# Performance work log

Measured on AMD Instinct MI355X. Metric: run time of the kernel, lower is better.

The kernel has to match this reference:

```python
import jax, jax.numpy as jnp
import numpy as np

B, H, K, V = 64, 32, 128, 128


def setup_inputs() -> dict:
    key = jax.random.key(0)
    ks = jax.random.split(key, 7)
    q = jax.random.normal(ks[0], (B, 1, H, K), dtype=jnp.float32)
    k = jax.random.normal(ks[1], (B, 1, H, K), dtype=jnp.float32)
    v = jax.random.normal(ks[2], (B, 1, H, V), dtype=jnp.float32)
    # a = -kappa, b = kappa*a_gate in RWKV-7; plain gaussians suffice for a math reference
    a = jax.random.normal(ks[3], (B, 1, H, K), dtype=jnp.float32)
    b = jax.random.normal(ks[4], (B, 1, H, K), dtype=jnp.float32)
    # gk is a log-decay: negative so exp(gk) in (0, 1]
    gk = -jnp.abs(jax.random.normal(ks[5], (B, 1, H, K), dtype=jnp.float32)) * 0.1
    h0 = jax.random.normal(ks[6], (B, H, K, V), dtype=jnp.float32) * 0.1
    return {"q": q, "k": k, "v": v, "a": a, "b": b, "gk": gk, "h0": h0}


def reference(q, k, v, a, b, gk, h0):
    """RWKV-7 DPLR single-step (T=1) decode recurrence, per (batch, head):
      g     = exp(gk)                                # [K] decay
      s     = a^T H0                                 # [V]
      t     = (q*g)^T H0                             # [V]
      alpha = q . b ; beta = q . k                   # scalars
      o     = t + alpha*s + beta*v                   # [V]
      Ht    = diag(g) H0 + b s^T + k v^T             # [K,V]
    Mirrors dplr_decode_t1_kernel_streamK exactly (fp32 accumulation).
    """
    qf = q[:, 0].astype(jnp.float32)   # [B,H,K]
    kf = k[:, 0].astype(jnp.float32)
    af = a[:, 0].astype(jnp.float32)
    bf = b[:, 0].astype(jnp.float32)
    vf = v[:, 0].astype(jnp.float32)   # [B,H,V]
    g = jnp.exp(gk[:, 0].astype(jnp.float32))  # [B,H,K]
    hf = h0.astype(jnp.float32)        # [B,H,K,V]

    s = jnp.einsum('bhk,bhkv->bhv', af, hf)
    t = jnp.einsum('bhk,bhkv->bhv', qf * g, hf)
    alpha = jnp.sum(qf * bf, axis=-1, keepdims=True)  # [B,H,1]
    beta = jnp.sum(qf * kf, axis=-1, keepdims=True)   # [B,H,1]
    o = t + alpha * s + beta * vf                      # [B,H,V]

    ht = g[..., None] * hf + bf[..., None] * s[:, :, None, :] + kf[..., None] * vf[:, :, None, :]
    return o[:, None].astype(v.dtype), ht.astype(h0.dtype)
```

## Files before the change

### kernel.cpp

```cpp
#include <hip/hip_runtime.h>


#define KD 128
#define VD 128
#define BH_TOTAL 2048
#define WPB 4
#define NBLK (BH_TOTAL/WPB)
#define RKEEP 16
#define NSTRM (64 - RKEEP)

typedef float f32x4 __attribute__((ext_vector_type(4)));

__global__ __launch_bounds__(256, 2) void dplr_decode_wave_kernel(
    const float* __restrict__ q_,  const float* __restrict__ k_,
    const float* __restrict__ v_,  const float* __restrict__ a_,
    const float* __restrict__ b_,  const float* __restrict__ gk_,
    const float* __restrict__ h0_, float* __restrict__ out_)
{
    const int tid  = threadIdx.x;
    const int wid  = tid >> 6;
    const int lane = tid & 63;
    const int bh   = blockIdx.x * WPB + wid;
    const int half = lane >> 5;
    const int c4   = (lane & 31) * 4;

    const size_t vec_off = (size_t)bh * KD;
    const size_t h_off   = (size_t)bh * (KD * VD);

    __shared__ float aL[WPB][2][64], qgL[WPB][2][64], gL[WPB][2][64],
                     bL[WPB][2][64], kL[WPB][2][64];

    const float q_lo = q_[vec_off + lane],  q_hi = q_[vec_off + lane + 64];
    const float b_lo = b_[vec_off + lane],  b_hi = b_[vec_off + lane + 64];
    const float k_lo = k_[vec_off + lane],  k_hi = k_[vec_off + lane + 64];
    const float a_lo = a_[vec_off + lane],  a_hi = a_[vec_off + lane + 64];
    const float g_lo = expf(gk_[vec_off + lane]);
    const float g_hi = expf(gk_[vec_off + lane + 64]);

    {
        const int p  = lane & 1;
        const int m0 = lane >> 1;
        aL [wid][p][m0] = a_lo;        aL [wid][p][m0 + 32] = a_hi;
        qgL[wid][p][m0] = q_lo * g_lo; qgL[wid][p][m0 + 32] = q_hi * g_hi;
        gL [wid][p][m0] = g_lo;        gL [wid][p][m0 + 32] = g_hi;
        bL [wid][p][m0] = b_lo;        bL [wid][p][m0 + 32] = b_hi;
        kL [wid][p][m0] = k_lo;        kL [wid][p][m0 + 32] = k_hi;
    }

    float alpha = q_lo * b_lo + q_hi * b_hi;
    float beta  = q_lo * k_lo + q_hi * k_hi;
#pragma unroll
    for (int o = 32; o > 0; o >>= 1) {
        alpha += __shfl_xor(alpha, o, 64);
        beta  += __shfl_xor(beta,  o, 64);
    }

    const f32x4 v4 = *(const f32x4*)(v_ + vec_off + c4);

    const float* hp = h0_ + h_off + (size_t)half * VD + c4;

    f32x4 sp = {0.f, 0.f, 0.f, 0.f};
    f32x4 tp = {0.f, 0.f, 0.f, 0.f};
    f32x4 Hk[RKEEP];

#pragma unroll
    for (int mb = 0; mb < NSTRM / 4; ++mb) {
        const f32x4 av = *(const f32x4*)&aL [wid][half][mb * 4];
        const f32x4 qv = *(const f32x4*)&qgL[wid][half][mb * 4];
#pragma unroll
        for (int e = 0; e < 4; ++e) {
            const int m = mb * 4 + e;
            const f32x4 h = *(const f32x4*)(hp + (size_t)m * 256);
            sp += av[e] * h;
            tp += qv[e] * h;
        }
    }
#pragma unroll
    for (int j = 0; j < RKEEP; ++j) {
        const int m = NSTRM + j;
        Hk[j] = *(const f32x4*)(hp + (size_t)m * 256);
        sp += aL [wid][half][m] * Hk[j];
        tp += qgL[wid][half][m] * Hk[j];
    }

    f32x4 s4, t4;
#pragma unroll
    for (int e = 0; e < 4; ++e) {
        s4[e] = sp[e] + __shfl_xor(sp[e], 32, 64);
        t4[e] = tp[e] + __shfl_xor(tp[e], 32, 64);
    }

    if (half == 0) {
        const f32x4 o4 = t4 + alpha * s4 + beta * v4;
        *(f32x4*)(out_ + (size_t)bh * VD + c4) = o4;
    }

    float* op = out_ + (size_t)BH_TOTAL * VD + h_off + (size_t)half * VD + c4;
#pragma unroll
    for (int mb = 0; mb < NSTRM / 4; ++mb) {
        const f32x4 gv = *(const f32x4*)&gL[wid][half][mb * 4];
        const f32x4 bv = *(const f32x4*)&bL[wid][half][mb * 4];
        const f32x4 kv = *(const f32x4*)&kL[wid][half][mb * 4];
#pragma unroll
        for (int e = 0; e < 4; ++e) {
            const int m = mb * 4 + e;
            const f32x4 h = __builtin_nontemporal_load((const f32x4*)(hp + (size_t)m * 256));
            const f32x4 o4 = gv[e] * h + bv[e] * s4 + kv[e] * v4;
            __builtin_nontemporal_store(o4, (f32x4*)(op + (size_t)m * 256));
        }
    }
#pragma unroll
    for (int j = 0; j < RKEEP; ++j) {
        const int m = NSTRM + j;
        const f32x4 o4 = gL[wid][half][m] * Hk[j] + bL[wid][half][m] * s4
                       + kL[wid][half][m] * v4;
        __builtin_nontemporal_store(o4, (f32x4*)(op + (size_t)m * 256));
    }
}

extern "C" void kernel_launch(void* const* d_in, const int* in_sizes, int n_in,
                              void* d_out, int out_size, void* d_ws, size_t ws_size,
                              hipStream_t stream) {
    const float* q  = (const float*)d_in[0];
    const float* k  = (const float*)d_in[1];
    const float* v  = (const float*)d_in[2];
    const float* a  = (const float*)d_in[3];
    const float* b  = (const float*)d_in[4];
    const float* gk = (const float*)d_in[5];
    const float* h0 = (const float*)d_in[6];
    float* out = (float*)d_out;

    dplr_decode_wave_kernel<<<NBLK, 256, 0, stream>>>(q, k, v, a, b, gk, h0, out);
}
```

Measured before the change: 254.4 us.

## Split each head's state across a whole block by column groups

Each (batch, head) pair now gets its own 256-thread block instead of one wave. Each wave owns 32 value columns, and 8 row groups per wave cover 16 rows each; the s and t partial sums are reduced with a three-step shuffle. The register cache of the last 16 rows is removed, so the second pass re-reads all of H0 with ordinary cached loads instead of nontemporal ones, and the occupancy hint is raised. The aim is more memory parallelism and occupancy, at the cost of re-reading the full state, which now depends on L2 hits.

New measurement: 254.7 us. About the same (+0.1%).

```diff
diff --git a/kernel.cpp b/kernel.cpp
--- a/kernel.cpp
+++ b/kernel.cpp
@@ -5,13 +5,11 @@
 #define VD 128
 #define BH_TOTAL 2048
 #define WPB 4
-#define NBLK (BH_TOTAL/WPB)
-#define RKEEP 16
-#define NSTRM (64 - RKEEP)
+#define NBLK BH_TOTAL
 
 typedef float f32x4 __attribute__((ext_vector_type(4)));
 
-__global__ __launch_bounds__(256, 2) void dplr_decode_wave_kernel(
+__global__ __launch_bounds__(256, 6) void dplr_decode_colsplit_kernel(
     const float* __restrict__ q_,  const float* __restrict__ k_,
     const float* __restrict__ v_,  const float* __restrict__ a_,
     const float* __restrict__ b_,  const float* __restrict__ gk_,
@@ -20,15 +18,16 @@
     const int tid  = threadIdx.x;
     const int wid  = tid >> 6;
     const int lane = tid & 63;
-    const int bh   = blockIdx.x * WPB + wid;
-    const int half = lane >> 5;
-    const int c4   = (lane & 31) * 4;
+    const int bh   = blockIdx.x;
+    const int rg   = lane >> 3;
+    const int l8   = lane & 7;
+    const int c4   = wid * 32 + l8 * 4;
 
     const size_t vec_off = (size_t)bh * KD;
     const size_t h_off   = (size_t)bh * (KD * VD);
 
-    __shared__ float aL[WPB][2][64], qgL[WPB][2][64], gL[WPB][2][64],
-                     bL[WPB][2][64], kL[WPB][2][64];
+    __shared__ float aL[WPB][8][16], qgL[WPB][8][16], gL[WPB][8][16],
+                     bL[WPB][8][16], kL[WPB][8][16];
 
     const float q_lo = q_[vec_off + lane],  q_hi = q_[vec_off + lane + 64];
     const float b_lo = b_[vec_off + lane],  b_hi = b_[vec_off + lane + 64];
@@ -38,13 +37,13 @@
     const float g_hi = expf(gk_[vec_off + lane + 64]);
 
     {
-        const int p  = lane & 1;
-        const int m0 = lane >> 1;
-        aL [wid][p][m0] = a_lo;        aL [wid][p][m0 + 32] = a_hi;
-        qgL[wid][p][m0] = q_lo * g_lo; qgL[wid][p][m0 + 32] = q_hi * g_hi;
-        gL [wid][p][m0] = g_lo;        gL [wid][p][m0 + 32] = g_hi;
-        bL [wid][p][m0] = b_lo;        bL [wid][p][m0 + 32] = b_hi;
-        kL [wid][p][m0] = k_lo;        kL [wid][p][m0 + 32] = k_hi;
+        const int p  = lane & 7;
+        const int m0 = lane >> 3;
+        aL [wid][p][m0] = a_lo;        aL [wid][p][m0 + 8] = a_hi;
+        qgL[wid][p][m0] = q_lo * g_lo; qgL[wid][p][m0 + 8] = q_hi * g_hi;
+        gL [wid][p][m0] = g_lo;        gL [wid][p][m0 + 8] = g_hi;
+        bL [wid][p][m0] = b_lo;        bL [wid][p][m0 + 8] = b_hi;
+        kL [wid][p][m0] = k_lo;        kL [wid][p][m0 + 8] = k_hi;
     }
 
     float alpha = q_lo * b_lo + q_hi * b_hi;
@@ -57,64 +56,56 @@
 
     const f32x4 v4 = *(const f32x4*)(v_ + vec_off + c4);
 
-    const float* hp = h0_ + h_off + (size_t)half * VD + c4;
+    const float* hp = h0_ + h_off + (size_t)rg * VD + c4;
 
     f32x4 sp = {0.f, 0.f, 0.f, 0.f};
     f32x4 tp = {0.f, 0.f, 0.f, 0.f};
-    f32x4 Hk[RKEEP];
-
 #pragma unroll
-    for (int mb = 0; mb < NSTRM / 4; ++mb) {
-        const f32x4 av = *(const f32x4*)&aL [wid][half][mb * 4];
-        const f32x4 qv = *(const f32x4*)&qgL[wid][half][mb * 4];
+    for (int mb = 0; mb < 4; ++mb) {
+        const f32x4 av = *(const f32x4*)&aL [wid][rg][mb * 4];
+        const f32x4 qv = *(const f32x4*)&qgL[wid][rg][mb * 4];
 #pragma unroll
         for (int e = 0; e < 4; ++e) {
             const int m = mb * 4 + e;
-            const f32x4 h = *(const f32x4*)(hp + (size_t)m * 256);
+            const f32x4 h = *(const f32x4*)(hp + (size_t)m * (8 * VD));
             sp += av[e] * h;
             tp += qv[e] * h;
         }
-    }
-#pragma unroll
-    for (int j = 0; j < RKEEP; ++j) {
-        const int m = NSTRM + j;
-        Hk[j] = *(const f32x4*)(hp + (size_t)m * 256);
-        sp += aL [wid][half][m] * Hk[j];
-        tp += qgL[wid][half][m] * Hk[j];
     }
 
     f32x4 s4, t4;
 #pragma unroll
     for (int e = 0; e < 4; ++e) {
-        s4[e] = sp[e] + __shfl_xor(sp[e], 32, 64);
-        t4[e] = tp[e] + __shfl_xor(tp[e], 32, 64);
+        float x = sp[e];
+        x += __shfl_xor(x,  8, 64);
+        x += __shfl_xor(x, 16, 64);
+        x += __shfl_xor(x, 32, 64);
+        s4[e] = x;
+        float y = tp[e];
+        y += __shfl_xor(y,  8, 64);
+        y += __shfl_xor(y, 16, 64);
+        y += __shfl_xor(y, 32, 64);
+        t4[e] = y;
     }
 
-    if (half == 0) {
+    if (rg == 0) {
         const f32x4 o4 = t4 + alpha * s4 + beta * v4;
         *(f32x4*)(out_ + (size_t)bh * VD + c4) = o4;
     }
 
-    float* op = out_ + (size_t)BH_TOTAL * VD + h_off + (size_t)half * VD + c4;
+    float* op = out_ + (size_t)BH_TOTAL * VD + h_off + (size_t)rg * VD + c4;
 #pragma unroll
-    for (int mb = 0; mb < NSTRM / 4; ++mb) {
-        const f32x4 gv = *(const f32x4*)&gL[wid][half][mb * 4];
-        const f32x4 bv = *(const f32x4*)&bL[wid][half][mb * 4];
-        const f32x4 kv = *(const f32x4*)&kL[wid][half][mb * 4];
+    for (int mb = 0; mb < 4; ++mb) {
+        const f32x4 gv = *(const f32x4*)&gL[wid][rg][mb * 4];
+        const f32x4 bv = *(const f32x4*)&bL[wid][rg][mb * 4];
+        const f32x4 kv = *(const f32x4*)&kL[wid][rg][mb * 4];
 #pragma unroll
         for (int e = 0; e < 4; ++e) {
             const int m = mb * 4 + e;
-            const f32x4 h = __builtin_nontemporal_load((const f32x4*)(hp + (size_t)m * 256));
+            const f32x4 h = *(const f32x4*)(hp + (size_t)m * (8 * VD));
             const f32x4 o4 = gv[e] * h + bv[e] * s4 + kv[e] * v4;
-            __builtin_nontemporal_store(o4, (f32x4*)(op + (size_t)m * 256));
+            __builtin_nontemporal_store(o4, (f32x4*)(op + (size_t)m * (8 * VD)));
         }
-    }
-#pragma unroll
-    for (int j = 0; j < RKEEP; ++j) {
-        const int m = NSTRM + j;
-        const f32x4 o4 = gL[wid][half][m] * Hk[j] + bL[wid][half][m] * s4
-                       + kL[wid][half][m] * v4;
-        __builtin_nontemporal_store(o4, (f32x4*)(op + (size_t)m * 256));
     }
 }
 
@@ -130,5 +121,5 @@
     const float* h0 = (const float*)d_in[6];
     float* out = (float*)d_out;
 
-    dplr_decode_wave_kernel<<<NBLK, 256, 0, stream>>>(q, k, v, a, b, gk, h0, out);
+    dplr_decode_colsplit_kernel<<<NBLK, 256, 0, stream>>>(q, k, v, a, b, gk, h0, out);
 }
```

## Keep entire H0 slice in registers to read state once

Applied to the files above, without the earlier changes.

Each lane now loads all 64 of its H0 float4 chunks into registers up front, before the small vector loads, and uses them for both the s/t reductions and the Ht update. This removes the second global read of H0 that the previous partial-keep scheme paid for 48 of 64 chunks. The cost is 256 VGPRs per lane just for H, with launch bounds lowered to one block per CU, so occupancy drops and register spills are possible. An empty asm barrier pins the loaded values so the loads are all issued early.

Result: no change. 253.4 us (-0.4%).

```diff
diff --git a/kernel.cpp b/kernel.cpp
--- a/kernel.cpp
+++ b/kernel.cpp
@@ -6,12 +6,11 @@
 #define BH_TOTAL 2048
 #define WPB 4
 #define NBLK (BH_TOTAL/WPB)
-#define RKEEP 16
-#define NSTRM (64 - RKEEP)
+#define NCHUNK 64
 
 typedef float f32x4 __attribute__((ext_vector_type(4)));
 
-__global__ __launch_bounds__(256, 2) void dplr_decode_wave_kernel(
+__global__ __launch_bounds__(256, 1) void dplr_decode_fullkeep_kernel(
     const float* __restrict__ q_,  const float* __restrict__ k_,
     const float* __restrict__ v_,  const float* __restrict__ a_,
     const float* __restrict__ b_,  const float* __restrict__ gk_,
@@ -29,6 +28,13 @@
 
     __shared__ float aL[WPB][2][64], qgL[WPB][2][64], gL[WPB][2][64],
                      bL[WPB][2][64], kL[WPB][2][64];
+
+    f32x4 Hk[NCHUNK];
+    const float* hp = h0_ + h_off + (size_t)half * VD + c4;
+#pragma unroll
+    for (int m = 0; m < NCHUNK; ++m) {
+        Hk[m] = *(const f32x4*)(hp + (size_t)m * 256);
+    }
 
     const float q_lo = q_[vec_off + lane],  q_hi = q_[vec_off + lane + 64];
     const float b_lo = b_[vec_off + lane],  b_hi = b_[vec_off + lane + 64];
@@ -57,30 +63,22 @@
 
     const f32x4 v4 = *(const f32x4*)(v_ + vec_off + c4);
 
-    const float* hp = h0_ + h_off + (size_t)half * VD + c4;
+#pragma unroll
+    for (int m = 0; m < NCHUNK; ++m) {
+        asm volatile("" : "+v"(Hk[m]));
+    }
 
     f32x4 sp = {0.f, 0.f, 0.f, 0.f};
     f32x4 tp = {0.f, 0.f, 0.f, 0.f};
-    f32x4 Hk[RKEEP];
-
 #pragma unroll
-    for (int mb = 0; mb < NSTRM / 4; ++mb) {
+    for (int mb = 0; mb < NCHUNK / 4; ++mb) {
         const f32x4 av = *(const f32x4*)&aL [wid][half][mb * 4];
         const f32x4 qv = *(const f32x4*)&qgL[wid][half][mb * 4];
 #pragma unroll
         for (int e = 0; e < 4; ++e) {
-            const int m = mb * 4 + e;
-            const f32x4 h = *(const f32x4*)(hp + (size_t)m * 256);
-            sp += av[e] * h;
-            tp += qv[e] * h;
+            sp += av[e] * Hk[mb * 4 + e];
+            tp += qv[e] * Hk[mb * 4 + e];
         }
-    }
-#pragma unroll
-    for (int j = 0; j < RKEEP; ++j) {
-        const int m = NSTRM + j;
-        Hk[j] = *(const f32x4*)(hp + (size_t)m * 256);
-        sp += aL [wid][half][m] * Hk[j];
-        tp += qgL[wid][half][m] * Hk[j];
     }
 
     f32x4 s4, t4;
@@ -97,24 +95,16 @@
 
     float* op = out_ + (size_t)BH_TOTAL * VD + h_off + (size_t)half * VD + c4;
 #pragma unroll
-    for (int mb = 0; mb < NSTRM / 4; ++mb) {
+    for (int mb = 0; mb < NCHUNK / 4; ++mb) {
         const f32x4 gv = *(const f32x4*)&gL[wid][half][mb * 4];
         const f32x4 bv = *(const f32x4*)&bL[wid][half][mb * 4];
         const f32x4 kv = *(const f32x4*)&kL[wid][half][mb * 4];
 #pragma unroll
         for (int e = 0; e < 4; ++e) {
             const int m = mb * 4 + e;
-            const f32x4 h = __builtin_nontemporal_load((const f32x4*)(hp + (size_t)m * 256));
-            const f32x4 o4 = gv[e] * h + bv[e] * s4 + kv[e] * v4;
+            const f32x4 o4 = gv[e] * Hk[m] + bv[e] * s4 + kv[e] * v4;
             __builtin_nontemporal_store(o4, (f32x4*)(op + (size_t)m * 256));
         }
-    }
-#pragma unroll
-    for (int j = 0; j < RKEEP; ++j) {
-        const int m = NSTRM + j;
-        const f32x4 o4 = gL[wid][half][m] * Hk[j] + bL[wid][half][m] * s4
-                       + kL[wid][half][m] * v4;
-        __builtin_nontemporal_store(o4, (f32x4*)(op + (size_t)m * 256));
     }
 }
 
@@ -130,5 +120,5 @@
     const float* h0 = (const float*)d_in[6];
     float* out = (float*)d_out;
 
-    dplr_decode_wave_kernel<<<NBLK, 256, 0, stream>>>(q, k, v, a, b, gk, h0, out);
+    dplr_decode_fullkeep_kernel<<<NBLK, 256, 0, stream>>>(q, k, v, a, b, gk, h0, out);
 }
```
